# Performance work log

Measured on AMD Instinct MI355X. Metric: run time of the kernel, lower is better.

The kernel has to match this reference:

```python
import jax, jax.numpy as jnp
import numpy as np

N_NODES = 50000
N_EDGES = 800000
HEADS = 4
NEG_SLOPE = 0.2  # PyG GATConv default leaky_relu slope
EPS = 1e-16      # PyG softmax denominator epsilon


def setup_inputs() -> dict:
    key = jax.random.key(0)
    ks = jax.random.split(key, 20)
    g = lambda k, shape, s=0.1: jax.random.normal(k, shape, dtype=jnp.float32) * s
    inp = {
        "x": g(ks[0], (N_NODES, 7), 1.0),
        "edge_index": jax.random.randint(ks[1], (2, N_EDGES), 0, N_NODES, dtype=jnp.int32),
        # encoder MLP 7 -> 64 -> 64
        "enc_w1": g(ks[2], (7, 64)), "enc_b1": jnp.zeros((64,), jnp.float32),
        "enc_w2": g(ks[3], (64, 64)), "enc_b2": jnp.zeros((64,), jnp.float32),
        # GATConv 1: in=64, heads=4, out_per_head=64, concat -> 256
        "g1_w": g(ks[4], (64, HEADS * 64)),
        "g1_as": g(ks[5], (HEADS, 64)), "g1_ad": g(ks[6], (HEADS, 64)),
        "g1_b": jnp.zeros((HEADS * 64,), jnp.float32),
        # GATConv 2: in=256, heads=4, out_per_head=16, concat -> 64
        "g2_w": g(ks[7], (256, HEADS * 16)),
        "g2_as": g(ks[8], (HEADS, 16)), "g2_ad": g(ks[9], (HEADS, 16)),
        "g2_b": jnp.zeros((HEADS * 16,), jnp.float32),
        # decoder MLP 64 -> 64 -> 4
        "dec_w1": g(ks[10], (64, 64)), "dec_b1": jnp.zeros((64,), jnp.float32),
        "dec_w2": g(ks[11], (64, 4)), "dec_b2": jnp.zeros((4,), jnp.float32),
    }
    return inp


def gat_conv(x, src, dst, n_nodes, W, a_src, a_dst, bias):
    """PyG GATConv (concat=True, self-loops already appended to src/dst)."""
    H, C = a_src.shape
    h = (x @ W).reshape(n_nodes, H, C)                      # [N,H,C]
    alpha_src = jnp.einsum('nhc,hc->nh', h, a_src)          # [N,H]
    alpha_dst = jnp.einsum('nhc,hc->nh', h, a_dst)          # [N,H]
    e = jax.nn.leaky_relu(alpha_src[src] + alpha_dst[dst], NEG_SLOPE)  # [E,H]
    # segment softmax over each destination node's incoming edges
    m = jax.ops.segment_max(e, dst, num_segments=n_nodes)   # [N,H]
    e = jnp.exp(e - m[dst])
    denom = jax.ops.segment_sum(e, dst, num_segments=n_nodes)
    alpha = e / (denom[dst] + EPS)                          # [E,H]
    msg = h[src] * alpha[:, :, None]                        # [E,H,C]
    out = jax.ops.segment_sum(msg, dst, num_segments=n_nodes)  # [N,H,C]
    return out.reshape(n_nodes, H * C) + bias


def reference(x, edge_index, enc_w1, enc_b1, enc_w2, enc_b2,
              g1_w, g1_as, g1_ad, g1_b, g2_w, g2_as, g2_ad, g2_b,
              dec_w1, dec_b1, dec_w2, dec_b2):
    n = x.shape[0]
    loop = jnp.arange(n, dtype=edge_index.dtype)
    src = jnp.concatenate([edge_index[0], loop])  # add self loops (PyG default)
    dst = jnp.concatenate([edge_index[1], loop])

    h = jax.nn.relu(x @ enc_w1 + enc_b1) @ enc_w2 + enc_b2   # encoder
    h = gat_conv(h, src, dst, n, g1_w, g1_as, g1_ad, g1_b)   # GAT layer 1
    h = jax.nn.elu(h)                                        # activation (dropout off in eval)
    h = gat_conv(h, src, dst, n, g2_w, g2_as, g2_ad, g2_b)   # GAT layer 2 (last: no act)
    out = jax.nn.relu(h @ dec_w1 + dec_b1) @ dec_w2 + dec_b2  # decoder
    return out
```

## Files before the change

### kernel.cpp

```cpp
#include <hip/hip_runtime.h>
#include <hip/hip_bf16.h>

#define N_NODES 50000
#define N_EDGES 800000
#define ET_EDGES 850000
#define HEADS 4
#define ENC_BLOCKS 1563

#define BSHIFT 8
#define NBUK 196
#define BCAP 6144
#define EB_PER_BLOCK 4096
#define EB_BLOCKS 208

#define G12NB 782
#define NAGG_BLOCKS 3125

#define W1HI 0
#define W1LO 16384
#define W2HI 32768
#define W2LO 49152
#define GCHI 65536
#define GCLO 69632
#define WT_TOTAL 73728

typedef __attribute__((ext_vector_type(8))) short bf16x8;
typedef __attribute__((ext_vector_type(4))) float f32x4;
#define MFMA16(a, b, c) __builtin_amdgcn_mfma_f32_16x16x32_bf16((a), (b), (c), 0, 0, 0)

__device__ __forceinline__ float lrelu(float v) { return v > 0.f ? v : 0.2f * v; }

__device__ __forceinline__ unsigned short f2bf(float f) {
    unsigned int u = __float_as_uint(f);
    u = (u + 0x7FFFu + ((u >> 16) & 1u)) >> 16;
    return (unsigned short)u;
}
__device__ __forceinline__ float bf2f(unsigned short h) {
    return __uint_as_float((unsigned int)h << 16);
}

__device__ __forceinline__ void edge_sd(const int* __restrict__ ei, int e, int& s, int& d) {
    if (e < N_EDGES) { s = ei[e]; d = ei[N_EDGES + e]; }
    else { s = d = e - N_EDGES; }
}

__global__ __launch_bounds__(256) void zerofold_kernel(
    int* __restrict__ bcur,
    const float* __restrict__ g1w, const float* __restrict__ g1as, const float* __restrict__ g1ad,
    float* __restrict__ wsf, float* __restrict__ wdf,
    const float* __restrict__ g2w, const float* __restrict__ g2as, const float* __restrict__ g2ad,
    unsigned short* __restrict__ wtb) {
    int b = blockIdx.x;
    int tid = threadIdx.x;
    if (b == 0) {
        if (tid < NBUK) bcur[tid] = 0;
        return;
    }
    if (b == 1) {
        int h = tid >> 6, k = tid & 63;
        float as_acc = 0.f, ad_acc = 0.f;
        #pragma unroll 8
        for (int c = 0; c < 64; ++c) {
            float w = g1w[k * 256 + h * 64 + c];
            as_acc += w * g1as[h * 64 + c];
            ad_acc += w * g1ad[h * 64 + c];
        }
        wsf[tid] = as_acc;
        wdf[tid] = ad_acc;
        return;
    }
    if (b < 18) {
        int gidx0 = (b - 2) * 2048 + tid * 8;
        #pragma unroll
        for (int u = 0; u < 8; ++u) {
            int idx = gidx0 + u;
            float w;
            int dst;
            if (idx < 16384) {
                int h = idx >> 12, q = (idx >> 6) & 63, k = idx & 63;
                w = g1w[k * 256 + h * 64 + q];
                dst = W1HI + idx;
            } else {
                int i2 = idx - 16384;
                int c = i2 >> 8, K = i2 & 255;
                w = g2w[K * 64 + c];
                dst = W2HI + i2;
            }
            unsigned short hi = f2bf(w);
            unsigned short lo = f2bf(w - bf2f(hi));
            wtb[dst] = hi;
            wtb[dst + 16384] = lo;
        }
        return;
    }
    {
        int gidx0 = (b - 18) * 2048 + tid * 8;
        #pragma unroll
        for (int u = 0; u < 8; ++u) {
            int idx = gidx0 + u;
            int j = idx >> 8, K = idx & 255;
            float acc = 0.f;
            if (j < 8) {
                int h = j >> 1;
                const float* gv = (j & 1) ? g2ad : g2as;
                #pragma unroll
                for (int cc = 0; cc < 16; ++cc)
                    acc += g2w[K * 64 + h * 16 + cc] * gv[h * 16 + cc];
            }
            unsigned short hi = f2bf(acc);
            unsigned short lo = f2bf(acc - bf2f(hi));
            wtb[GCHI + idx] = hi;
            wtb[GCLO + idx] = lo;
        }
        return;
    }
}

__global__ __launch_bounds__(256) void mega_kernel(
    const int* __restrict__ ei, int* __restrict__ bcur, int* __restrict__ ebuf,
    const float* __restrict__ x, const float* __restrict__ w1, const float* __restrict__ b1,
    const float* __restrict__ w2, const float* __restrict__ b2,
    const float* __restrict__ wsf, const float* __restrict__ wdf,
    unsigned short* __restrict__ henc, float* __restrict__ as1, float* __restrict__ ad1) {
    __shared__ union {
        struct { int es[EB_PER_BLOCK]; int ed[EB_PER_BLOCK]; int h[NBUK]; int base[NBUK]; } buk;
        struct { float w2[4096]; float t[32][64]; float xx[32][8]; float he[32][65]; float wf[8 * 65]; } enc;
    } u;
    int tid = threadIdx.x;
    if (blockIdx.x < EB_BLOCKS) {
        for (int i = tid; i < NBUK; i += 256) u.buk.h[i] = 0;
        int e0 = blockIdx.x * EB_PER_BLOCK;
        __syncthreads();
        #pragma unroll
        for (int r = 0; r < EB_PER_BLOCK / 256; ++r) {
            int i = r * 256 + tid;
            int e = e0 + i;
            if (e < ET_EDGES) {
                int s, d; edge_sd(ei, e, s, d);
                u.buk.es[i] = s;
                u.buk.ed[i] = d;
                atomicAdd(&u.buk.h[d >> BSHIFT], 1);
            } else {
                u.buk.ed[i] = -1;
            }
        }
        __syncthreads();
        for (int i = tid; i < NBUK; i += 256) {
            int c = u.buk.h[i];
            u.buk.base[i] = c ? atomicAdd(bcur + i, c) : 0;
            u.buk.h[i] = 0;
        }
        __syncthreads();
        #pragma unroll
        for (int r = 0; r < EB_PER_BLOCK / 256; ++r) {
            int i = r * 256 + tid;
            int d = u.buk.ed[i];
            if (d >= 0) {
                int b = d >> BSHIFT;
                int off = atomicAdd(&u.buk.h[b], 1);
                ebuf[b * BCAP + u.buk.base[b] + off] = ((d & 255) << 16) | u.buk.es[i];
            }
        }
        return;
    }
    int node0 = (blockIdx.x - EB_BLOCKS) * 32;
    for (int i = tid; i < 4096; i += 256) u.enc.w2[i] = w2[i];
    for (int i = tid; i < 224; i += 256) {
        int src = node0 * 7 + i;
        u.enc.xx[i / 7][i % 7] = (src < N_NODES * 7) ? x[src] : 0.f;
    }
    for (int i = tid; i < 512; i += 256) {
        int g = i >> 6, k = i & 63;
        int h = g & 3;
        u.enc.wf[g * 65 + k] = (g < 4) ? wsf[h * 64 + k] : wdf[h * 64 + k];
    }
    int c = tid & 63;
    int mg = tid >> 6;
    float w1c[7];
    #pragma unroll
    for (int k = 0; k < 7; ++k) w1c[k] = w1[k * 64 + c];
    float b1c = b1[c];
    __syncthreads();
    #pragma unroll
    for (int m = 0; m < 8; ++m) {
        int nn = mg * 8 + m;
        float a = b1c;
        #pragma unroll
        for (int k = 0; k < 7; ++k) a += u.enc.xx[nn][k] * w1c[k];
        u.enc.t[nn][c] = fmaxf(a, 0.f);
    }
    __syncthreads();
    float acc[8];
    float b2c = b2[c];
    #pragma unroll
    for (int m = 0; m < 8; ++m) acc[m] = b2c;
    #pragma unroll 4
    for (int k = 0; k < 64; ++k) {
        float w = u.enc.w2[k * 64 + c];
        #pragma unroll
        for (int m = 0; m < 8; ++m) acc[m] += u.enc.t[mg * 8 + m][k] * w;
    }
    #pragma unroll
    for (int m = 0; m < 8; ++m) {
        int nn = mg * 8 + m;
        int node = node0 + nn;
        u.enc.he[nn][c] = acc[m];
        if (node < N_NODES) henc[node * 64 + c] = f2bf(acc[m]);
    }
    __syncthreads();
    {
        int nn = tid >> 3, r = tid & 7;
        int node = node0 + nn;
        const float* wf = u.enc.wf + r * 65;
        float sum = 0.f;
        #pragma unroll 8
        for (int k = 0; k < 64; ++k) sum += u.enc.he[nn][k] * wf[k];
        if (node < N_NODES) {
            int hh = r & 3;
            if (r < 4) as1[node * 4 + hh] = sum;
            else       ad1[node * 4 + hh] = sum;
        }
    }
}

__global__ __launch_bounds__(256) void bucket_csr_kernel(
    const int* __restrict__ ebuf, const int* __restrict__ bcur,
    int* __restrict__ rowbeg, int* __restrict__ degarr, int* __restrict__ csr_src) {
    __shared__ int s_deg[256];
    __shared__ int s_cur[256];
    __shared__ int s_w[4];
    int b = blockIdx.x;
    int tid = threadIdx.x;
    s_deg[tid] = 0;
    int cnt = bcur[b];
    int base = b * BCAP;
    const int* eb = ebuf + base;
    int node0 = b << BSHIFT;
    __syncthreads();
    for (int i = tid; i < cnt; i += 256) atomicAdd(&s_deg[eb[i] >> 16], 1);
    __syncthreads();
    int v = s_deg[tid];
    int lane = tid & 63, w = tid >> 6;
    int xv = v;
    #pragma unroll
    for (int off = 1; off < 64; off <<= 1) {
        int t = __shfl_up(xv, off);
        if (lane >= off) xv += t;
    }
    if (lane == 63) s_w[w] = xv;
    __syncthreads();
    if (tid == 0) {
        int a = 0;
        #pragma unroll
        for (int j = 0; j < 4; ++j) { int t = s_w[j]; s_w[j] = a; a += t; }
    }
    __syncthreads();
    int excl = xv - v + s_w[w];
    s_cur[tid] = excl;
    int node = node0 + tid;
    if (node < N_NODES) {
        rowbeg[node] = base + excl;
        degarr[node] = v;
    }
    __syncthreads();
    for (int i = tid; i < cnt; i += 256) {
        int p = eb[i];
        int pos = atomicAdd(&s_cur[p >> 16], 1);
        csr_src[base + pos] = p & 0xFFFF;
    }
}

__global__ __launch_bounds__(256) void aggregate1_kernel(
    const int* __restrict__ rowbeg, const int* __restrict__ degarr, const int* __restrict__ csr_src,
    const float* __restrict__ as, const float* __restrict__ ad,
    const unsigned short* __restrict__ henc, unsigned short* __restrict__ agg) {
    __shared__ int    ls[16][17];
    __shared__ float4 lp[16][17];
    int tid = threadIdx.x;
    int gg = tid >> 4, lane16 = tid & 15;
    int n = blockIdx.x * 16 + gg;
    if (n >= N_NODES) return;
    int base = rowbeg[n];
    int deg  = degarr[n];
    float4 add = *(const float4*)(ad + n * 4);

    float4 l = make_float4(0.f, 0.f, 0.f, 0.f);
    float acc[4][4];
    #pragma unroll
    for (int f = 0; f < 4; ++f)
        #pragma unroll
        for (int h = 0; h < 4; ++h) acc[f][h] = 0.f;

    for (int c0 = 0; c0 < deg; c0 += 16) {
        int j = c0 + lane16;
        int s = 0;
        float4 p = make_float4(0.f, 0.f, 0.f, 0.f);
        if (j < deg) {
            s = csr_src[base + j];
            float4 a = *(const float4*)(as + s * 4);
            p.x = __expf(lrelu(a.x + add.x));
            p.y = __expf(lrelu(a.y + add.y));
            p.z = __expf(lrelu(a.z + add.z));
            p.w = __expf(lrelu(a.w + add.w));
            l.x += p.x; l.y += p.y; l.z += p.z; l.w += p.w;
        }
        ls[gg][lane16] = s;
        lp[gg][lane16] = p;
        int cnt = min(16, deg - c0);
        const int*    lsw = ls[gg];
        const float4* lpw = lp[gg];
        int e = 0;
        for (; e + 4 <= cnt; e += 4) {
            ushort4 r0 = *(const ushort4*)(henc + lsw[e+0] * 64 + lane16 * 4);
            ushort4 r1 = *(const ushort4*)(henc + lsw[e+1] * 64 + lane16 * 4);
            ushort4 r2 = *(const ushort4*)(henc + lsw[e+2] * 64 + lane16 * 4);
            ushort4 r3 = *(const ushort4*)(henc + lsw[e+3] * 64 + lane16 * 4);
            float4 p0 = lpw[e+0], p1 = lpw[e+1], p2 = lpw[e+2], p3 = lpw[e+3];
            #define ACC1(r, pp) { \
                float v0 = bf2f(r.x), v1 = bf2f(r.y), v2 = bf2f(r.z), v3 = bf2f(r.w); \
                acc[0][0] += v0*pp.x; acc[0][1] += v0*pp.y; acc[0][2] += v0*pp.z; acc[0][3] += v0*pp.w; \
                acc[1][0] += v1*pp.x; acc[1][1] += v1*pp.y; acc[1][2] += v1*pp.z; acc[1][3] += v1*pp.w; \
                acc[2][0] += v2*pp.x; acc[2][1] += v2*pp.y; acc[2][2] += v2*pp.z; acc[2][3] += v2*pp.w; \
                acc[3][0] += v3*pp.x; acc[3][1] += v3*pp.y; acc[3][2] += v3*pp.z; acc[3][3] += v3*pp.w; }
            ACC1(r0, p0) ACC1(r1, p1) ACC1(r2, p2) ACC1(r3, p3)
        }
        for (; e < cnt; ++e) {
            ushort4 r = *(const ushort4*)(henc + lsw[e] * 64 + lane16 * 4);
            float4 pp = lpw[e];
            ACC1(r, pp)
        }
    }
    #pragma unroll
    for (int off = 1; off < 16; off <<= 1) {
        l.x += __shfl_xor(l.x, off);
        l.y += __shfl_xor(l.y, off);
        l.z += __shfl_xor(l.z, off);
        l.w += __shfl_xor(l.w, off);
    }
    float inv[4];
    inv[0] = 1.f / (l.x + 1e-16f);
    inv[1] = 1.f / (l.y + 1e-16f);
    inv[2] = 1.f / (l.z + 1e-16f);
    inv[3] = 1.f / (l.w + 1e-16f);
    const size_t PL = (size_t)N_NODES * 64;
    #pragma unroll
    for (int h = 0; h < 4; ++h) {
        ushort4 o;
        o.x = f2bf(acc[0][h] * inv[h]);
        o.y = f2bf(acc[1][h] * inv[h]);
        o.z = f2bf(acc[2][h] * inv[h]);
        o.w = f2bf(acc[3][h] * inv[h]);
        *(ushort4*)(agg + h * PL + (size_t)n * 64 + lane16 * 4) = o;
    }
}

__global__ __launch_bounds__(512, 1) void gemm12_kernel(
    const unsigned short* __restrict__ agg, const unsigned short* __restrict__ wtb,
    const float* __restrict__ g1b, unsigned short* __restrict__ h2,
    float* __restrict__ as2, float* __restrict__ ad2) {
    __shared__ unsigned short sw[40960];
    __shared__ unsigned short s1[16384];
    int tid = threadIdx.x;
    int node0 = blockIdx.x * 64;
    int lane = tid & 63, w = tid >> 6;
    int lrow = lane & 15, g = lane >> 4;
    int rw = w & 3, hp = w >> 2;
    const size_t PL = (size_t)N_NODES * 64;

    {
        const uint4* src = (const uint4*)(wtb + W1HI);
        uint4* dst = (uint4*)sw;
        #pragma unroll
        for (int r = 0; r < 8; ++r) {
            int i = r * 512 + tid;
            dst[i ^ ((i >> 3) & 7)] = src[i];
        }
    }
    int arow = node0 + rw * 16 + lrow;
    if (arow >= N_NODES) arow = N_NODES - 1;
    bf16x8 aF[2][2];
    #pragma unroll
    for (int hh = 0; hh < 2; ++hh)
        #pragma unroll
        for (int ks = 0; ks < 2; ++ks)
            aF[hh][ks] = *(const bf16x8*)(agg + (size_t)(hp * 2 + hh) * PL + (size_t)arow * 64 + ks * 32 + g * 8);
    float bb[2][4];
    #pragma unroll
    for (int hh = 0; hh < 2; ++hh)
        #pragma unroll
        for (int qt = 0; qt < 4; ++qt)
            bb[hh][qt] = g1b[(hp * 2 + hh) * 64 + qt * 16 + lrow];
    __syncthreads();

    f32x4 acc1[2][4];
    #pragma unroll
    for (int hh = 0; hh < 2; ++hh)
        #pragma unroll
        for (int qt = 0; qt < 4; ++qt) acc1[hh][qt] = (f32x4){0.f, 0.f, 0.f, 0.f};
    #pragma unroll
    for (int hh = 0; hh < 2; ++hh) {
        int h = hp * 2 + hh;
        #pragma unroll
        for (int ks = 0; ks < 2; ++ks) {
            #pragma unroll
            for (int qt = 0; qt < 4; ++qt) {
                int q = qt * 16 + lrow;
                int byt = (h * 8192 + q * 128 + ks * 64 + g * 16) ^ ((q & 7) << 4);
                bf16x8 bH = *(const bf16x8*)((char*)sw + byt);
                bf16x8 bL = *(const bf16x8*)((char*)sw + byt + 32768);
                acc1[hh][qt] = MFMA16(aF[hh][ks], bH, acc1[hh][qt]);
                acc1[hh][qt] = MFMA16(aF[hh][ks], bL, acc1[hh][qt]);
            }
        }
    }
    #pragma unroll
    for (int hh = 0; hh < 2; ++hh) {
        int h = hp * 2 + hh;
        #pragma unroll
        for (int qt = 0; qt < 4; ++qt) {
            int col = h * 64 + qt * 16 + lrow;
            #pragma unroll
            for (int i = 0; i < 4; ++i) {
                int r = rw * 16 + g * 4 + i;
                float t = acc1[hh][qt][i] + bb[hh][qt];
                t = t > 0.f ? t : (__expf(t) - 1.f);
                int byt = (r * 512 + col * 2) ^ ((r & 7) << 4);
                *(unsigned short*)((char*)s1 + byt) = f2bf(t);
            }
        }
    }
    __syncthreads();
    {
        const uint4* src = (const uint4*)(wtb + W2HI);
        uint4* dst = (uint4*)sw;
        #pragma unroll
        for (int r = 0; r < 10; ++r) {
            int i = r * 512 + tid;
            dst[i ^ ((i >> 5) & 7)] = src[i];
        }
    }
    __syncthreads();
    f32x4 acc2[2];
    f32x4 accg = (f32x4){0.f, 0.f, 0.f, 0.f};
    acc2[0] = (f32x4){0.f, 0.f, 0.f, 0.f};
    acc2[1] = (f32x4){0.f, 0.f, 0.f, 0.f};
    int rloc = rw * 16 + lrow;
    int rx = (rloc & 7) << 4;
    #pragma unroll
    for (int ks = 0; ks < 8; ++ks) {
        int kb = ks * 64 + g * 16;
        bf16x8 aF2 = *(const bf16x8*)((char*)s1 + ((rloc * 512 + kb) ^ rx));
        #pragma unroll
        for (int qt = 0; qt < 2; ++qt) {
            int c = (hp * 2 + qt) * 16 + lrow;
            int byt = (c * 512 + kb) ^ ((c & 7) << 4);
            bf16x8 bH = *(const bf16x8*)((char*)sw + byt);
            bf16x8 bL = *(const bf16x8*)((char*)sw + byt + 32768);
            acc2[qt] = MFMA16(aF2, bH, acc2[qt]);
            acc2[qt] = MFMA16(aF2, bL, acc2[qt]);
        }
        if (hp == 0) {
            int byt = 65536 + ((lrow * 512 + kb) ^ ((lrow & 7) << 4));
            bf16x8 gH = *(const bf16x8*)((char*)sw + byt);
            bf16x8 gL = *(const bf16x8*)((char*)sw + byt + 8192);
            accg = MFMA16(aF2, gH, accg);
            accg = MFMA16(aF2, gL, accg);
        }
    }
    #pragma unroll
    for (int i = 0; i < 4; ++i) {
        int node = node0 + rw * 16 + g * 4 + i;
        if (node < N_NODES) {
            #pragma unroll
            for (int qt = 0; qt < 2; ++qt)
                h2[(size_t)node * 64 + (hp * 2 + qt) * 16 + lrow] = f2bf(acc2[qt][i]);
            if (hp == 0 && lrow < 8) {
                float v = accg[i];
                int hh = lrow >> 1;
                if (lrow & 1) ad2[node * 4 + hh] = v;
                else          as2[node * 4 + hh] = v;
            }
        }
    }
}

__global__ __launch_bounds__(256) void aggregate2_kernel(
    const int* __restrict__ rowbeg, const int* __restrict__ degarr, const int* __restrict__ csr_src,
    const float* __restrict__ as, const float* __restrict__ ad,
    const unsigned short* __restrict__ h, float* __restrict__ out) {
    __shared__ int    ls[16][17];
    __shared__ float4 lp[16][17];
    int tid = threadIdx.x;
    int gg = tid >> 4, lane16 = tid & 15;
    int n = blockIdx.x * 16 + gg;
    if (n >= N_NODES) return;
    int base = rowbeg[n];
    int deg  = degarr[n];
    int head = lane16 >> 2;
    float4 add = *(const float4*)(ad + n * 4);

    float4 l = make_float4(0.f, 0.f, 0.f, 0.f);
    float acc[4];
    acc[0] = acc[1] = acc[2] = acc[3] = 0.f;

    for (int c0 = 0; c0 < deg; c0 += 16) {
        int j = c0 + lane16;
        int s = 0;
        float4 p = make_float4(0.f, 0.f, 0.f, 0.f);
        if (j < deg) {
            s = csr_src[base + j];
            float4 a = *(const float4*)(as + s * 4);
            p.x = __expf(lrelu(a.x + add.x));
            p.y = __expf(lrelu(a.y + add.y));
            p.z = __expf(lrelu(a.z + add.z));
            p.w = __expf(lrelu(a.w + add.w));
            l.x += p.x; l.y += p.y; l.z += p.z; l.w += p.w;
        }
        ls[gg][lane16] = s;
        lp[gg][lane16] = p;
        int cnt = min(16, deg - c0);
        const int*   lsw = ls[gg];
        const float* lpf = (const float*)lp[gg];
        int e = 0;
        for (; e + 4 <= cnt; e += 4) {
            ushort4 r0 = *(const ushort4*)(h + lsw[e+0] * 64 + lane16 * 4);
            ushort4 r1 = *(const ushort4*)(h + lsw[e+1] * 64 + lane16 * 4);
            ushort4 r2 = *(const ushort4*)(h + lsw[e+2] * 64 + lane16 * 4);
            ushort4 r3 = *(const ushort4*)(h + lsw[e+3] * 64 + lane16 * 4);
            float p0 = lpf[(e+0) * 4 + head];
            float p1 = lpf[(e+1) * 4 + head];
            float p2 = lpf[(e+2) * 4 + head];
            float p3 = lpf[(e+3) * 4 + head];
            acc[0] += bf2f(r0.x)*p0 + bf2f(r1.x)*p1 + bf2f(r2.x)*p2 + bf2f(r3.x)*p3;
            acc[1] += bf2f(r0.y)*p0 + bf2f(r1.y)*p1 + bf2f(r2.y)*p2 + bf2f(r3.y)*p3;
            acc[2] += bf2f(r0.z)*p0 + bf2f(r1.z)*p1 + bf2f(r2.z)*p2 + bf2f(r3.z)*p3;
            acc[3] += bf2f(r0.w)*p0 + bf2f(r1.w)*p1 + bf2f(r2.w)*p2 + bf2f(r3.w)*p3;
        }
        for (; e < cnt; ++e) {
            ushort4 r = *(const ushort4*)(h + lsw[e] * 64 + lane16 * 4);
            float pe = lpf[e * 4 + head];
            acc[0] += bf2f(r.x) * pe;
            acc[1] += bf2f(r.y) * pe;
            acc[2] += bf2f(r.z) * pe;
            acc[3] += bf2f(r.w) * pe;
        }
    }
    #pragma unroll
    for (int off = 1; off < 16; off <<= 1) {
        l.x += __shfl_xor(l.x, off);
        l.y += __shfl_xor(l.y, off);
        l.z += __shfl_xor(l.z, off);
        l.w += __shfl_xor(l.w, off);
    }
    float lh = (head == 0) ? l.x : (head == 1) ? l.y : (head == 2) ? l.z : l.w;
    float inv = 1.f / (lh + 1e-16f);
    float4 o;
    o.x = acc[0] * inv; o.y = acc[1] * inv; o.z = acc[2] * inv; o.w = acc[3] * inv;
    *(float4*)(out + (size_t)n * 64 + lane16 * 4) = o;
}

__global__ __launch_bounds__(256) void decoder32_kernel(
    const float* __restrict__ hin, const float* __restrict__ gb,
    const float* __restrict__ w1, const float* __restrict__ b1,
    const float* __restrict__ w2, const float* __restrict__ b2, float* __restrict__ out) {
    __shared__ float s_w1[4096];
    __shared__ float s_w2[256];
    __shared__ float s_h[32][64];
    __shared__ float s_t[32][64];
    int tid = threadIdx.x;
    int node0 = blockIdx.x * 32;
    for (int i = tid; i < 4096; i += 256) s_w1[i] = w1[i];
    if (tid < 256) s_w2[tid] = w2[tid];
    for (int i = tid; i < 2048; i += 256) {
        int nn = i >> 6, k = i & 63;
        int node = node0 + nn;
        s_h[nn][k] = (node < N_NODES ? hin[(size_t)node * 64 + k] : 0.f) + gb[k];
    }
    __syncthreads();
    int c = tid & 63;
    int mg = tid >> 6;
    float b1c = b1[c];
    float acc[8];
    #pragma unroll
    for (int m = 0; m < 8; ++m) acc[m] = b1c;
    #pragma unroll 4
    for (int k = 0; k < 64; ++k) {
        float w = s_w1[k * 64 + c];
        #pragma unroll
        for (int m = 0; m < 8; ++m) acc[m] += s_h[mg * 8 + m][k] * w;
    }
    #pragma unroll
    for (int m = 0; m < 8; ++m) s_t[mg * 8 + m][c] = fmaxf(acc[m], 0.f);
    __syncthreads();
    if (tid < 128) {
        int m = tid >> 2, j = tid & 3;
        int node = node0 + m;
        if (node < N_NODES) {
            float a = b2[j];
            #pragma unroll 16
            for (int k = 0; k < 64; ++k) a += s_t[m][k] * s_w2[k * 4 + j];
            out[node * 4 + j] = a;
        }
    }
}

extern "C" void kernel_launch(void* const* d_in, const int* in_sizes, int n_in,
                              void* d_out, int out_size, void* d_ws, size_t ws_size,
                              hipStream_t stream) {
    const float* x      = (const float*)d_in[0];
    const int*   ei     = (const int*)d_in[1];
    const float* enc_w1 = (const float*)d_in[2];
    const float* enc_b1 = (const float*)d_in[3];
    const float* enc_w2 = (const float*)d_in[4];
    const float* enc_b2 = (const float*)d_in[5];
    const float* g1_w   = (const float*)d_in[6];
    const float* g1_as  = (const float*)d_in[7];
    const float* g1_ad  = (const float*)d_in[8];
    const float* g1_b   = (const float*)d_in[9];
    const float* g2_w   = (const float*)d_in[10];
    const float* g2_as  = (const float*)d_in[11];
    const float* g2_ad  = (const float*)d_in[12];
    const float* g2_b   = (const float*)d_in[13];
    const float* dec_w1 = (const float*)d_in[14];
    const float* dec_b1 = (const float*)d_in[15];
    const float* dec_w2 = (const float*)d_in[16];
    const float* dec_b2 = (const float*)d_in[17];

    const int N = N_NODES;

    float* ws   = (float*)d_ws;
    unsigned short* henc = (unsigned short*)ws;
    unsigned short* wtb  = (unsigned short*)(ws + 1700000);
    unsigned short* agg  = (unsigned short*)(ws + 3200000);
    unsigned short* h2   = (unsigned short*)(ws + 16000000);
    float* out2 = ws + 19200000;
    unsigned short* out1 = (unsigned short*)(ws + 22400000);
    float* as1  = ws + 35200000;
    float* ad1  = as1 + 200000;
    float* as2  = ad1 + 200000;
    float* ad2  = as2 + 200000;
    float* wsf  = ad2 + 200000;
    float* wdf  = wsf + 256;
    int*   ebuf = (int*)out1;
    int*   ib      = (int*)(ws + 36001024);
    int*   bcur    = ib;
    int*   rowbeg  = ib + 256;
    int*   degarr  = ib + 50432;
    int*   csr_src = ib + 100608;

    zerofold_kernel<<<20, 256, 0, stream>>>(bcur, g1_w, g1_as, g1_ad, wsf, wdf,
                                            g2_w, g2_as, g2_ad, wtb);
    mega_kernel<<<EB_BLOCKS + ENC_BLOCKS, 256, 0, stream>>>(
        ei, bcur, ebuf, x, enc_w1, enc_b1, enc_w2, enc_b2, wsf, wdf, henc, as1, ad1);
    bucket_csr_kernel<<<NBUK, 256, 0, stream>>>(ebuf, bcur, rowbeg, degarr, csr_src);

    aggregate1_kernel<<<NAGG_BLOCKS, 256, 0, stream>>>(rowbeg, degarr, csr_src, as1, ad1, henc, agg);
    gemm12_kernel<<<G12NB, 512, 0, stream>>>(agg, wtb, g1_b, h2, as2, ad2);

    aggregate2_kernel<<<NAGG_BLOCKS, 256, 0, stream>>>(rowbeg, degarr, csr_src, as2, ad2, h2, out2);

    decoder32_kernel<<<(N + 31) / 32, 256, 0, stream>>>(out2, g2_b, dec_w1, dec_b1, dec_w2, dec_b2, (float*)d_out);
}
```

Baseline: 238.9 us.

## Fuse GAT layer-2 aggregation with decoder MLP into one kernel

The second aggregation kernel now applies the bias and runs the 64->64->4 decoder MLP per node directly, using shared-memory copies of the decoder weights and a 16-lane shuffle reduction for the final projection. This removes the fp32 intermediate write and re-read of the aggregated features and one kernel launch. In exchange, every aggregation block loads the 16KB decoder weight matrix and uses more shared memory, which may lower occupancy for the latency-bound gather.

Measured after the change: 229.6 us, median of 2. 1.04x faster.

```diff
diff --git a/kernel.cpp b/kernel.cpp
--- a/kernel.cpp
+++ b/kernel.cpp
@@ -484,13 +484,27 @@
     }
 }
 
-__global__ __launch_bounds__(256) void aggregate2_kernel(
+__global__ __launch_bounds__(256) void aggdec2_kernel(
     const int* __restrict__ rowbeg, const int* __restrict__ degarr, const int* __restrict__ csr_src,
     const float* __restrict__ as, const float* __restrict__ ad,
-    const unsigned short* __restrict__ h, float* __restrict__ out) {
+    const unsigned short* __restrict__ h, const float* __restrict__ gb,
+    const float* __restrict__ w1, const float* __restrict__ b1,
+    const float* __restrict__ w2, const float* __restrict__ b2,
+    float* __restrict__ out) {
     __shared__ int    ls[16][17];
     __shared__ float4 lp[16][17];
+    __shared__ float  s_w1[4096];
+    __shared__ float  s_w2[256];
+    __shared__ float  s_v[16][68];
     int tid = threadIdx.x;
+    #pragma unroll
+    for (int r = 0; r < 4; ++r) {
+        int i = r * 256 + tid;
+        *(float4*)(s_w1 + i * 4) = *(const float4*)(w1 + i * 4);
+    }
+    if (tid < 64) *(float4*)(s_w2 + tid * 4) = *(const float4*)(w2 + tid * 4);
+    __syncthreads();
+
     int gg = tid >> 4, lane16 = tid & 15;
     int n = blockIdx.x * 16 + gg;
     if (n >= N_NODES) return;
@@ -554,53 +568,39 @@
     }
     float lh = (head == 0) ? l.x : (head == 1) ? l.y : (head == 2) ? l.z : l.w;
     float inv = 1.f / (lh + 1e-16f);
-    float4 o;
-    o.x = acc[0] * inv; o.y = acc[1] * inv; o.z = acc[2] * inv; o.w = acc[3] * inv;
-    *(float4*)(out + (size_t)n * 64 + lane16 * 4) = o;
-}
-
-__global__ __launch_bounds__(256) void decoder32_kernel(
-    const float* __restrict__ hin, const float* __restrict__ gb,
-    const float* __restrict__ w1, const float* __restrict__ b1,
-    const float* __restrict__ w2, const float* __restrict__ b2, float* __restrict__ out) {
-    __shared__ float s_w1[4096];
-    __shared__ float s_w2[256];
-    __shared__ float s_h[32][64];
-    __shared__ float s_t[32][64];
-    int tid = threadIdx.x;
-    int node0 = blockIdx.x * 32;
-    for (int i = tid; i < 4096; i += 256) s_w1[i] = w1[i];
-    if (tid < 256) s_w2[tid] = w2[tid];
-    for (int i = tid; i < 2048; i += 256) {
-        int nn = i >> 6, k = i & 63;
-        int node = node0 + nn;
-        s_h[nn][k] = (node < N_NODES ? hin[(size_t)node * 64 + k] : 0.f) + gb[k];
-    }
-    __syncthreads();
-    int c = tid & 63;
-    int mg = tid >> 6;
-    float b1c = b1[c];
-    float acc[8];
-    #pragma unroll
-    for (int m = 0; m < 8; ++m) acc[m] = b1c;
-    #pragma unroll 4
+    int c0v = lane16 * 4;
+    float4 vv;
+    vv.x = acc[0] * inv + gb[c0v + 0];
+    vv.y = acc[1] * inv + gb[c0v + 1];
+    vv.z = acc[2] * inv + gb[c0v + 2];
+    vv.w = acc[3] * inv + gb[c0v + 3];
+    *(float4*)(&s_v[gg][c0v]) = vv;
+    float t0 = b1[c0v + 0], t1 = b1[c0v + 1], t2 = b1[c0v + 2], t3 = b1[c0v + 3];
+    #pragma unroll 8
     for (int k = 0; k < 64; ++k) {
-        float w = s_w1[k * 64 + c];
-        #pragma unroll
-        for (int m = 0; m < 8; ++m) acc[m] += s_h[mg * 8 + m][k] * w;
-    }
-    #pragma unroll
-    for (int m = 0; m < 8; ++m) s_t[mg * 8 + m][c] = fmaxf(acc[m], 0.f);
-    __syncthreads();
-    if (tid < 128) {
-        int m = tid >> 2, j = tid & 3;
-        int node = node0 + m;
-        if (node < N_NODES) {
-            float a = b2[j];
-            #pragma unroll 16
-            for (int k = 0; k < 64; ++k) a += s_t[m][k] * s_w2[k * 4 + j];
-            out[node * 4 + j] = a;
-        }
+        float vk = s_v[gg][k];
+        float4 wv = *(const float4*)(s_w1 + k * 64 + c0v);
+        t0 += vk * wv.x; t1 += vk * wv.y; t2 += vk * wv.z; t3 += vk * wv.w;
+    }
+    t0 = fmaxf(t0, 0.f); t1 = fmaxf(t1, 0.f); t2 = fmaxf(t2, 0.f); t3 = fmaxf(t3, 0.f);
+    float4 w20 = *(const float4*)(s_w2 + (c0v + 0) * 4);
+    float4 w21 = *(const float4*)(s_w2 + (c0v + 1) * 4);
+    float4 w22 = *(const float4*)(s_w2 + (c0v + 2) * 4);
+    float4 w23 = *(const float4*)(s_w2 + (c0v + 3) * 4);
+    float o0 = t0 * w20.x + t1 * w21.x + t2 * w22.x + t3 * w23.x;
+    float o1 = t0 * w20.y + t1 * w21.y + t2 * w22.y + t3 * w23.y;
+    float o2 = t0 * w20.z + t1 * w21.z + t2 * w22.z + t3 * w23.z;
+    float o3 = t0 * w20.w + t1 * w21.w + t2 * w22.w + t3 * w23.w;
+    #pragma unroll
+    for (int off = 1; off < 16; off <<= 1) {
+        o0 += __shfl_xor(o0, off);
+        o1 += __shfl_xor(o1, off);
+        o2 += __shfl_xor(o2, off);
+        o3 += __shfl_xor(o3, off);
+    }
+    if (lane16 == 0) {
+        *(float4*)(out + (size_t)n * 4) =
+            make_float4(o0 + b2[0], o1 + b2[1], o2 + b2[2], o3 + b2[3]);
     }
 }
 
@@ -633,7 +633,6 @@
     unsigned short* wtb  = (unsigned short*)(ws + 1700000);
     unsigned short* agg  = (unsigned short*)(ws + 3200000);
     unsigned short* h2   = (unsigned short*)(ws + 16000000);
-    float* out2 = ws + 19200000;
     unsigned short* out1 = (unsigned short*)(ws + 22400000);
     float* as1  = ws + 35200000;
     float* ad1  = as1 + 200000;
@@ -657,7 +656,7 @@
     aggregate1_kernel<<<NAGG_BLOCKS, 256, 0, stream>>>(rowbeg, degarr, csr_src, as1, ad1, henc, agg);
     gemm12_kernel<<<G12NB, 512, 0, stream>>>(agg, wtb, g1_b, h2, as2, ad2);
 
-    aggregate2_kernel<<<NAGG_BLOCKS, 256, 0, stream>>>(rowbeg, degarr, csr_src, as2, ad2, h2, out2);
-
-    decoder32_kernel<<<(N + 31) / 32, 256, 0, stream>>>(out2, g2_b, dec_w1, dec_b1, dec_w2, dec_b2, (float*)d_out);
-}
+    aggdec2_kernel<<<NAGG_BLOCKS, 256, 0, stream>>>(rowbeg, degarr, csr_src, as2, ad2, h2,
+                                                    g2_b, dec_w1, dec_b1, dec_w2, dec_b2,
+                                                    (float*)d_out);
+}
```
